# Optimization experiments

Measured on AMD Instinct MI355X. Metric: run time of the kernel, lower is better.

Reference implementation:

```python
import jax, jax.numpy as jnp
import numpy as np

NUM_HEADS = 16
HEAD_DIM = 64
HIDDEN = NUM_HEADS * HEAD_DIM
LN_EPS = 1e-6


def setup_inputs() -> dict:
    key = jax.random.key(0)
    ks = jax.random.split(key, 5)
    B, T, H = 2, 2048, HIDDEN
    s = 1.0 / np.sqrt(H)
    return {
        "h": jax.random.normal(ks[0], (B, T, H), jnp.float32),
        "Wq": jax.random.normal(ks[1], (H, H), jnp.float32) * s,
        "bq": jnp.zeros((H,), jnp.float32),
        "Wk": jax.random.normal(ks[2], (H, H), jnp.float32) * s,
        "bk": jnp.zeros((H,), jnp.float32),
        "Wv": jax.random.normal(ks[3], (H, H), jnp.float32) * s,
        "bv": jnp.zeros((H,), jnp.float32),
        "Wo": jax.random.normal(ks[4], (H, H), jnp.float32) * s,
        "bo": jnp.zeros((H,), jnp.float32),
        "gamma": jnp.ones((H,), jnp.float32),
        "beta": jnp.zeros((H,), jnp.float32),
    }


def _split_heads(x):
    B, T, H = x.shape
    return x.reshape(B, T, NUM_HEADS, HEAD_DIM).transpose(0, 2, 1, 3)  # [B,h,T,d]


def reference(h, Wq, bq, Wk, bk, Wv, bv, Wo, bo, gamma, beta):
    # QKV projections (nn.Linear: x @ W^T + b)
    Q = _split_heads(h @ Wq.T + bq)
    K = _split_heads(h @ Wk.T + bk)
    V = _split_heads(h @ Wv.T + bv)
    scale = HEAD_DIM ** -0.5
    scores = jnp.einsum("bhqd,bhkd->bhqk", Q, K) * scale  # [B,h,T,T]
    attn = jax.nn.softmax(scores, axis=-1)
    ctx = jnp.einsum("bhqk,bhkd->bhqd", attn, V)          # [B,h,T,d]
    B, _, T, _ = ctx.shape
    ctx = ctx.transpose(0, 2, 1, 3).reshape(B, T, HIDDEN)
    out = ctx @ Wo.T + bo + h  # dropout is identity at eval
    # LayerNorm(eps=1e-6)
    mu = out.mean(-1, keepdims=True)
    var = jnp.mean((out - mu) ** 2, -1, keepdims=True)
    return (out - mu) * jax.lax.rsqrt(var + LN_EPS) * gamma + beta
```

## Files before the change

### kernel.cpp

```cpp
#include <hip/hip_runtime.h>
#include <hip/hip_bf16.h>

#define NH   16
#define HD   64
#define HID  1024
#define TSEQ 2048
#define BATCH 2
#define KSCALE 0.18033688011112042f

typedef __attribute__((ext_vector_type(4))) float f32x4;
typedef __attribute__((ext_vector_type(8))) short s16x8;
typedef __attribute__((ext_vector_type(4))) short s16x4;
typedef __attribute__((ext_vector_type(8))) _Float16 f16x8;
typedef __attribute__((ext_vector_type(4))) _Float16 f16x4;
typedef __attribute__((ext_vector_type(2))) _Float16 f16x2;

__device__ __forceinline__ unsigned short f2bf(float f) {
  union { float f; unsigned int u; } v; v.f = f;
  unsigned int r = v.u + 0x7fffu + ((v.u >> 16) & 1u);
  return (unsigned short)(r >> 16);
}
__device__ __forceinline__ float bf2f(unsigned short b) {
  union { unsigned int u; float f; } v; v.u = ((unsigned int)b) << 16; return v.f;
}

__device__ __forceinline__ void gll16(const void* g, void* l) {
  __builtin_amdgcn_global_load_lds(
      (const __attribute__((address_space(1))) unsigned int*)g,
      (__attribute__((address_space(3))) unsigned int*)l, 16, 0, 0);
}

#define WAITBAR(N)                                                      \
  do {                                                                  \
    __builtin_amdgcn_sched_barrier(0);                                  \
    asm volatile("s_waitcnt vmcnt(" #N ")\n\ts_barrier" ::: "memory");  \
  } while (0)

__global__ __launch_bounds__(256) void cast_all_k(
    const float* __restrict__ h,
    const float* __restrict__ w0, const float* __restrict__ w1,
    const float* __restrict__ w2, const float* __restrict__ w3,
    unsigned short* __restrict__ hb, unsigned short* __restrict__ wbase) {
  int i = blockIdx.x * 256 + threadIdx.x;
  const float* src; unsigned short* dst; int idx; float sc = 1.f;
  if (i < 1048576) { src = h; dst = hb; idx = i; }
  else {
    int idx4 = i - 1048576;
    int w = idx4 >> 18;
    idx = idx4 & 262143;
    src = (w == 0) ? w0 : (w == 1) ? w1 : (w == 2) ? w2 : w3;
    dst = wbase + (size_t)(idx4 - idx) * 4;
    if (w == 1) sc = KSCALE;
  }
  float4 v = ((const float4*)src)[idx];
  ushort4 o;
  o.x = f2bf(v.x * sc); o.y = f2bf(v.y * sc); o.z = f2bf(v.z * sc); o.w = f2bf(v.w * sc);
  ((ushort4*)dst)[idx] = o;
}

__global__ __launch_bounds__(256) void gemm_qkv(
    const unsigned short* __restrict__ hb,
    const unsigned short* __restrict__ wcat,
    const float* __restrict__ bq, const float* __restrict__ bk, const float* __restrict__ bv,
    unsigned short* __restrict__ qo, unsigned short* __restrict__ ko,
    unsigned short* __restrict__ vto) {
  __shared__ unsigned short Ash[4][128 * 32];
  __shared__ unsigned short Bsh[4][192 * 32];
  const int tid = threadIdx.x, lane = tid & 63, wave = tid >> 6;
  const int l15 = lane & 15, quad = lane >> 4;
  const int wr = wave >> 1, wc = wave & 1;
  const int bid = blockIdx.y * 16 + blockIdx.x;
  const int swz = (bid & 7) * 64 + (bid >> 3);
  const int bn = (swz & 15) * 192, bm = (swz >> 4) * 128;
  const char* Ab = (const char*)(hb + (size_t)bm * HID);
  const char* Bb = (const char*)(wcat + (size_t)bn * HID);
  const int off = tid * 16;
  const int r0 = off >> 6, c0 = off & 63;
  const size_t ga0 = (size_t)r0 * (HID * 2) + c0;
  const size_t ga1 = ga0 + (size_t)64  * (HID * 2);
  const size_t gb2 = ga0 + (size_t)128 * (HID * 2);
  const int lb0 = wave * 512;
  const int lb1 = 2048 + wave * 512;
  const int lb2 = 4096 + wave * 512;

  f32x4 acc[4][6];
#pragma unroll
  for (int i = 0; i < 4; ++i)
#pragma unroll
    for (int j = 0; j < 6; ++j) acc[i][j] = f32x4{0.f, 0.f, 0.f, 0.f};

  auto stage = [&](int bufi, int k0) {
    const size_t kb = (size_t)k0 * 2;
    gll16(Ab + ga0 + kb, &Ash[bufi][lb0]);
    gll16(Ab + ga1 + kb, &Ash[bufi][lb1]);
    gll16(Bb + ga0 + kb, &Bsh[bufi][lb0]);
    gll16(Bb + ga1 + kb, &Bsh[bufi][lb1]);
    gll16(Bb + gb2 + kb, &Bsh[bufi][lb2]);
  };
  auto compute = [&](int bufi) {
    s16x8 af[4], bfr[6];
#pragma unroll
    for (int i = 0; i < 4; ++i)
      af[i] = *(const s16x8*)(&Ash[bufi][(wr * 64 + i * 16 + l15) * 32 + quad * 8]);
#pragma unroll
    for (int j = 0; j < 6; ++j)
      bfr[j] = *(const s16x8*)(&Bsh[bufi][(wc * 96 + j * 16 + l15) * 32 + quad * 8]);
#pragma unroll
    for (int i = 0; i < 4; ++i)
#pragma unroll
      for (int j = 0; j < 6; ++j)
        acc[i][j] = __builtin_amdgcn_mfma_f32_16x16x32_bf16(af[i], bfr[j], acc[i][j], 0, 0, 0);
  };

  stage(0, 0);
  stage(1, 32);
  stage(2, 64);
  int cur = 0, pf = 3;
  const int NT = HID / 32;
  for (int t = 0; t < NT - 3; ++t) {
    WAITBAR(10);
    stage(pf, (t + 3) * 32);
    compute(cur);
    cur = (cur + 1) & 3;
    pf  = (pf + 1) & 3;
  }
  WAITBAR(10); compute(cur); cur = (cur + 1) & 3;
  WAITBAR(5);  compute(cur); cur = (cur + 1) & 3;
  WAITBAR(0);  compute(cur);

  const int rbase = bm + wr * 64;
#pragma unroll
  for (int j = 0; j < 6; ++j) {
    const int cg  = bn + wc * 96 + j * 16;
    const int mat = cg >> 10;
    const int coln = (cg & 1023) + l15;
    const int head = coln >> 6, d = coln & 63;
    if (mat == 2) {
      const float bb = bv[coln];
#pragma unroll
      for (int i = 0; i < 4; ++i) {
        const int row0 = rbase + i * 16 + quad * 4;
        const int bI = row0 >> 11, t0 = row0 & 2047;
        unsigned short o[4];
#pragma unroll
        for (int r = 0; r < 4; ++r) {
          _Float16 hv = (_Float16)(acc[i][j][r] + bb);
          o[r] = __builtin_bit_cast(unsigned short, hv);
        }
        *(s16x4*)(vto + ((size_t)((bI * NH + head) * HD + d)) * TSEQ + t0) = *(const s16x4*)o;
      }
    } else {
      unsigned short* dst = (mat == 0) ? qo : ko;
      const float bb = (mat == 0) ? bq[coln] : bk[coln] * KSCALE;
#pragma unroll
      for (int i = 0; i < 4; ++i) {
#pragma unroll
        for (int r = 0; r < 4; ++r) {
          const int row = rbase + i * 16 + quad * 4 + r;
          const int bI = row >> 11, t = row & 2047;
          dst[(((size_t)(bI * NH + head) * TSEQ) + t) * HD + d] = f2bf(acc[i][j][r] + bb);
        }
      }
    }
  }
}

__global__ __launch_bounds__(256) void gemm_out(
    const unsigned short* __restrict__ ctx, const unsigned short* __restrict__ wo,
    const float* __restrict__ bo, const float* __restrict__ hres,
    float* __restrict__ outf) {
  __shared__ unsigned short Ash[5][128 * 32];
  __shared__ unsigned short Bsh[5][64 * 32];
  const int tid = threadIdx.x, lane = tid & 63, wave = tid >> 6;
  const int l15 = lane & 15, quad = lane >> 4;
  const int wr = wave >> 1, wc = wave & 1;
  const int bid = blockIdx.y * 16 + blockIdx.x;
  const int swz = (bid & 7) * 64 + (bid >> 3);
  const int bn = (swz & 15) * 64, bm = (swz >> 4) * 128;
  const char* Ab = (const char*)(ctx + (size_t)bm * HID);
  const char* Bb = (const char*)(wo + (size_t)bn * HID);
  const int off = tid * 16;
  const int r0 = off >> 6, c0 = off & 63;
  const size_t ga0 = (size_t)r0 * (HID * 2) + c0;
  const size_t ga1 = ga0 + (size_t)64 * (HID * 2);
  const int lb0 = wave * 512, lb1 = 2048 + wave * 512;

  f32x4 acc[4][2];
#pragma unroll
  for (int i = 0; i < 4; ++i)
#pragma unroll
    for (int j = 0; j < 2; ++j) acc[i][j] = f32x4{0.f, 0.f, 0.f, 0.f};

  auto stage = [&](int bufi, int k0) {
    const size_t kb = (size_t)k0 * 2;
    gll16(Ab + ga0 + kb, &Ash[bufi][lb0]);
    gll16(Ab + ga1 + kb, &Ash[bufi][lb1]);
    gll16(Bb + ga0 + kb, &Bsh[bufi][lb0]);
  };
  auto compute = [&](int bufi) {
    s16x8 af[4], bfr[2];
#pragma unroll
    for (int i = 0; i < 4; ++i)
      af[i] = *(const s16x8*)(&Ash[bufi][(wr * 64 + i * 16 + l15) * 32 + quad * 8]);
#pragma unroll
    for (int j = 0; j < 2; ++j)
      bfr[j] = *(const s16x8*)(&Bsh[bufi][(wc * 32 + j * 16 + l15) * 32 + quad * 8]);
#pragma unroll
    for (int i = 0; i < 4; ++i)
#pragma unroll
      for (int j = 0; j < 2; ++j)
        acc[i][j] = __builtin_amdgcn_mfma_f32_16x16x32_bf16(af[i], bfr[j], acc[i][j], 0, 0, 0);
  };

  stage(0, 0);
  stage(1, 32);
  stage(2, 64);
  stage(3, 96);
  int cur = 0, pf = 4;
  const int NT = HID / 32;
  for (int t = 0; t < NT - 4; ++t) {
    WAITBAR(9);
    stage(pf, (t + 4) * 32);
    compute(cur);
    cur = (cur == 4) ? 0 : cur + 1;
    pf  = (pf  == 4) ? 0 : pf + 1;
  }
  WAITBAR(9); compute(cur); cur = (cur == 4) ? 0 : cur + 1;
  WAITBAR(6); compute(cur); cur = (cur == 4) ? 0 : cur + 1;
  WAITBAR(3); compute(cur); cur = (cur == 4) ? 0 : cur + 1;
  WAITBAR(0); compute(cur);

#pragma unroll
  for (int j = 0; j < 2; ++j) {
    const int col = bn + wc * 32 + j * 16 + l15;
    const float bb = bo[col];
#pragma unroll
    for (int i = 0; i < 4; ++i) {
#pragma unroll
      for (int r = 0; r < 4; ++r) {
        const int row = bm + wr * 64 + i * 16 + quad * 4 + r;
        const size_t o = (size_t)row * HID + col;
        outf[o] = acc[i][j][r] + bb + hres[o];
      }
    }
  }
}

__global__ __launch_bounds__(256, 2) void attn_k(
    const unsigned short* __restrict__ qb, const unsigned short* __restrict__ kb,
    const unsigned short* __restrict__ vt, unsigned short* __restrict__ ctx,
    int ntiles) {
  __shared__ unsigned short Ksh[2][64 * 72];
  __shared__ unsigned short Vsh[2][64 * 72];

  const int tid = threadIdx.x, lane = tid & 63, wave = tid >> 6;
  const int l15 = lane & 15, quad = lane >> 4;
  const int b = blockIdx.z;
  const int h = blockIdx.y, qt = blockIdx.x;
  const size_t ho = ((size_t)(b * NH + h)) * TSEQ * HD;
  const unsigned short* Qh = qb + ho;
  const unsigned short* Kh = kb + ho;
  const unsigned short* Vh = vt + ho;
  const int q0 = qt * 128 + wave * 32;

  s16x8 qf[2][2];
#pragma unroll
  for (int s = 0; s < 2; ++s)
#pragma unroll
    for (int ks = 0; ks < 2; ++ks)
      qf[s][ks] = *(const s16x8*)(Qh + (size_t)(q0 + s * 16 + l15) * HD + ks * 32 + quad * 8);

  f32x4 accO[4][2];
  f32x4 accR[2];
#pragma unroll
  for (int n2 = 0; n2 < 4; ++n2)
#pragma unroll
    for (int s = 0; s < 2; ++s) accO[n2][s] = f32x4{0.f, 0.f, 0.f, 0.f};
  accR[0] = accR[1] = f32x4{0.f, 0.f, 0.f, 0.f};
  const f16x8 vones = {(_Float16)1.f, (_Float16)1.f, (_Float16)1.f, (_Float16)1.f,
                       (_Float16)1.f, (_Float16)1.f, (_Float16)1.f, (_Float16)1.f};

  const int sr = tid >> 3, sc = (tid & 7) * 8;
  const int c = tid & 7;
  const int vwb = (c >> 2) * 32 + (c & 1) * 16 + ((c & 3) >> 1) * 4;
  s16x8 kreg[2], vreg[2];

  auto ldregs = [&](int kt) {
    const int k0n = kt * 64;
#pragma unroll
    for (int hf = 0; hf < 2; ++hf) {
      kreg[hf] = *(const s16x8*)(Kh + (size_t)(k0n + sr + hf * 32) * HD + sc);
      vreg[hf] = *(const s16x8*)(Vh + (size_t)(sr + hf * 32) * TSEQ + k0n + sc);
    }
  };
  auto wlds = [&](int bi) {
#pragma unroll
    for (int hf = 0; hf < 2; ++hf) {
      *(s16x8*)(Ksh[bi] + (sr + hf * 32) * 72 + sc) = kreg[hf];
      const s16x4* vh = (const s16x4*)&vreg[hf];
      *(s16x4*)(Vsh[bi] + (sr + hf * 32) * 72 + vwb)     = vh[0];
      *(s16x4*)(Vsh[bi] + (sr + hf * 32) * 72 + vwb + 8) = vh[1];
    }
  };

  f32x4 accS[2][4];
  f16x4 pP[2][4];

  auto qkt = [&](int bi) {
#pragma unroll
    for (int s = 0; s < 2; ++s)
#pragma unroll
      for (int n = 0; n < 4; ++n) accS[s][n] = f32x4{0.f, 0.f, 0.f, 0.f};
    __builtin_amdgcn_s_setprio(1);
#pragma unroll
    for (int ks = 0; ks < 2; ++ks) {
#pragma unroll
      for (int n = 0; n < 4; ++n) {
        s16x8 kf = *(const s16x8*)(Ksh[bi] + (n * 16 + l15) * 72 + ks * 32 + quad * 8);
#pragma unroll
        for (int s = 0; s < 2; ++s)
          accS[s][n] = __builtin_amdgcn_mfma_f32_16x16x32_bf16(kf, qf[s][ks], accS[s][n], 0, 0, 0);
      }
    }
    __builtin_amdgcn_s_setprio(0);
  };
  auto expp = [&]() {
#pragma unroll
    for (int s = 0; s < 2; ++s)
#pragma unroll
      for (int n = 0; n < 4; ++n) {
        float e0 = __builtin_amdgcn_exp2f(accS[s][n][0]);
        float e1 = __builtin_amdgcn_exp2f(accS[s][n][1]);
        float e2 = __builtin_amdgcn_exp2f(accS[s][n][2]);
        float e3 = __builtin_amdgcn_exp2f(accS[s][n][3]);
        f16x2 lo = __builtin_bit_cast(f16x2, __builtin_amdgcn_cvt_pkrtz(e0, e1));
        f16x2 hi = __builtin_bit_cast(f16x2, __builtin_amdgcn_cvt_pkrtz(e2, e3));
        pP[s][n] = f16x4{lo[0], lo[1], hi[0], hi[1]};
      }
  };
  auto pv = [&](int bi) {
    __builtin_amdgcn_s_setprio(1);
#pragma unroll
    for (int kk = 0; kk < 2; ++kk) {
      union { f16x4 h[2]; f16x8 v8; } u0, u1;
      u0.h[0] = pP[0][2 * kk]; u0.h[1] = pP[0][2 * kk + 1];
      u1.h[0] = pP[1][2 * kk]; u1.h[1] = pP[1][2 * kk + 1];
      accR[0] = __builtin_amdgcn_mfma_f32_16x16x32_f16(vones, u0.v8, accR[0], 0, 0, 0);
      accR[1] = __builtin_amdgcn_mfma_f32_16x16x32_f16(vones, u1.v8, accR[1], 0, 0, 0);
#pragma unroll
      for (int n2 = 0; n2 < 4; ++n2) {
        f16x8 vA = *(const f16x8*)(Vsh[bi] + (n2 * 16 + l15) * 72 + kk * 32 + quad * 8);
        accO[n2][0] = __builtin_amdgcn_mfma_f32_16x16x32_f16(vA, u0.v8, accO[n2][0], 0, 0, 0);
        accO[n2][1] = __builtin_amdgcn_mfma_f32_16x16x32_f16(vA, u1.v8, accO[n2][1], 0, 0, 0);
      }
    }
    __builtin_amdgcn_s_setprio(0);
  };

  ldregs(0);
  wlds(0);
  __syncthreads();
  if (ntiles > 1) ldregs(1);
  qkt(0);
  expp();

  for (int t = 0; t < ntiles - 1; ++t) {
    const int b0 = t & 1, b1 = (t + 1) & 1;
    __syncthreads();
    wlds(b1);
    __syncthreads();
    if (t + 2 < ntiles) ldregs(t + 2);
    qkt(b1);
    pv(b0);
    expp();
  }
  pv((ntiles - 1) & 1);

  float rsum[2] = {accR[0][0], accR[1][0]};

#pragma unroll
  for (int s = 0; s < 2; ++s) {
    const int t = q0 + s * 16 + l15;
    const float inv = 1.f / rsum[s];
#pragma unroll
    for (int n2 = 0; n2 < 4; ++n2) {
      const int d0 = n2 * 16 + quad * 4;
      unsigned short o[4];
#pragma unroll
      for (int r = 0; r < 4; ++r) o[r] = f2bf(accO[n2][s][r] * inv);
      *(s16x4*)(ctx + ((size_t)(b * TSEQ + t)) * HID + h * HD + d0) = *(const s16x4*)o;
    }
  }
}

__global__ __launch_bounds__(256) void ln_k(float* __restrict__ io,
                                            const float* __restrict__ gamma,
                                            const float* __restrict__ beta) {
  const int row = blockIdx.x, tid = threadIdx.x;
  float x[4]; float s = 0.f, s2 = 0.f;
#pragma unroll
  for (int i = 0; i < 4; ++i) {
    x[i] = io[(size_t)row * HID + tid + i * 256];
    s += x[i]; s2 += x[i] * x[i];
  }
#pragma unroll
  for (int off = 1; off < 64; off <<= 1) {
    s  += __shfl_xor(s, off, 64);
    s2 += __shfl_xor(s2, off, 64);
  }
  __shared__ float red[8];
  const int wave = tid >> 6;
  if ((tid & 63) == 0) { red[wave] = s; red[wave + 4] = s2; }
  __syncthreads();
  s  = red[0] + red[1] + red[2] + red[3];
  s2 = red[4] + red[5] + red[6] + red[7];
  const float mean = s * (1.f / HID);
  const float var  = s2 * (1.f / HID) - mean * mean;
  const float rstd = rsqrtf(var + 1e-6f);
#pragma unroll
  for (int i = 0; i < 4; ++i) {
    const int col = tid + i * 256;
    io[(size_t)row * HID + col] = (x[i] - mean) * rstd * gamma[col] + beta[col];
  }
}

extern "C" void kernel_launch(void* const* d_in, const int* in_sizes, int n_in,
                              void* d_out, int out_size, void* d_ws, size_t ws_size,
                              hipStream_t stream) {
  const float* h    = (const float*)d_in[0];
  const float* Wq   = (const float*)d_in[1];
  const float* bq   = (const float*)d_in[2];
  const float* Wk   = (const float*)d_in[3];
  const float* bk   = (const float*)d_in[4];
  const float* Wv   = (const float*)d_in[5];
  const float* bv   = (const float*)d_in[6];
  const float* Wo   = (const float*)d_in[7];
  const float* bo   = (const float*)d_in[8];
  const float* gamma = (const float*)d_in[9];
  const float* beta  = (const float*)d_in[10];
  float* out = (float*)d_out;

  unsigned short* hb   = (unsigned short*)d_ws;
  unsigned short* wqb  = hb  + 4194304;
  unsigned short* wkb  = wqb + 1048576;
  unsigned short* wvb  = wkb + 1048576;
  unsigned short* wob  = wvb + 1048576;
  unsigned short* qb   = wob + 1048576;
  unsigned short* kb   = qb  + 4194304;
  unsigned short* vtf  = kb  + 4194304;
  unsigned short* ctxb = hb;

  cast_all_k<<<8192, 256, 0, stream>>>(h, Wq, Wk, Wv, Wo, hb, wqb);
  gemm_qkv<<<dim3(16, 32), 256, 0, stream>>>(hb, wqb, bq, bk, bv, qb, kb, vtf);
  attn_k<<<dim3(TSEQ / 128, NH, BATCH), 256, 0, stream>>>(qb, kb, vtf, ctxb, 32);
  gemm_out<<<dim3(16, 32), 256, 0, stream>>>(ctxb, wob, bo, h, out);
  ln_k<<<4096, 256, 0, stream>>>(out, gamma, beta);
}
```

Baseline: 200.5 us.

## Fuse LayerNorm into out-projection via last-block counters; shrink attention query tile

The separate LayerNorm kernel is removed. Each gemm_out block now bumps a per-row-panel atomic counter, and the last of the 16 column blocks to finish applies LayerNorm over its 128 rows in place, with counters zeroed in the cast kernel. Separately, the attention query tile is halved from 128 to 64 rows (16 per wave instead of 32), doubling the grid and cutting per-wave registers. The trade is that each K/V tile loaded into LDS is now reused by half as many queries, and the fused LayerNorm runs serially inside the one block that finishes last for each panel.

```diff
diff --git a/kernel.cpp b/kernel.cpp
--- a/kernel.cpp
+++ b/kernel.cpp
@@ -40,7 +40,9 @@
     const float* __restrict__ h,
     const float* __restrict__ w0, const float* __restrict__ w1,
     const float* __restrict__ w2, const float* __restrict__ w3,
-    unsigned short* __restrict__ hb, unsigned short* __restrict__ wbase) {
+    unsigned short* __restrict__ hb, unsigned short* __restrict__ wbase,
+    unsigned int* __restrict__ cnt) {
+  if (blockIdx.x == 0 && threadIdx.x < 32) cnt[threadIdx.x] = 0;
   int i = blockIdx.x * 256 + threadIdx.x;
   const float* src; unsigned short* dst; int idx; float sc = 1.f;
   if (i < 1048576) { src = h; dst = hb; idx = i; }
@@ -168,7 +170,8 @@
 __global__ __launch_bounds__(256) void gemm_out(
     const unsigned short* __restrict__ ctx, const unsigned short* __restrict__ wo,
     const float* __restrict__ bo, const float* __restrict__ hres,
-    float* __restrict__ outf) {
+    float* __restrict__ outf, unsigned int* __restrict__ cnt,
+    const float* __restrict__ gamma, const float* __restrict__ beta) {
   __shared__ unsigned short Ash[5][128 * 32];
   __shared__ unsigned short Bsh[5][64 * 32];
   const int tid = threadIdx.x, lane = tid & 63, wave = tid >> 6;
@@ -244,6 +247,41 @@
       }
     }
   }
+
+  __threadfence();
+  __shared__ unsigned int lastf;
+  if (tid == 0)
+    lastf = (atomicAdd(&cnt[bm >> 7], 1u) == 15u) ? 1u : 0u;
+  __syncthreads();
+  if (!lastf) return;
+  __threadfence();
+  for (int rr = wave; rr < 128; rr += 4) {
+    float* rp = outf + (size_t)(bm + rr) * HID;
+    f32x4 x[4]; float s = 0.f, s2 = 0.f;
+#pragma unroll
+    for (int i = 0; i < 4; ++i) {
+      x[i] = *(const f32x4*)(rp + lane * 4 + i * 256);
+#pragma unroll
+      for (int r = 0; r < 4; ++r) { s += x[i][r]; s2 += x[i][r] * x[i][r]; }
+    }
+#pragma unroll
+    for (int o2 = 1; o2 < 64; o2 <<= 1) {
+      s  += __shfl_xor(s, o2, 64);
+      s2 += __shfl_xor(s2, o2, 64);
+    }
+    const float mean = s * (1.f / HID);
+    const float var  = s2 * (1.f / HID) - mean * mean;
+    const float rstd = rsqrtf(var + 1e-6f);
+#pragma unroll
+    for (int i = 0; i < 4; ++i) {
+      f32x4 g  = *(const f32x4*)(gamma + lane * 4 + i * 256);
+      f32x4 be = *(const f32x4*)(beta  + lane * 4 + i * 256);
+      f32x4 o;
+#pragma unroll
+      for (int r = 0; r < 4; ++r) o[r] = (x[i][r] - mean) * rstd * g[r] + be[r];
+      *(f32x4*)(rp + lane * 4 + i * 256) = o;
+    }
+  }
 }
 
 __global__ __launch_bounds__(256, 2) void attn_k(
@@ -261,22 +299,18 @@
   const unsigned short* Qh = qb + ho;
   const unsigned short* Kh = kb + ho;
   const unsigned short* Vh = vt + ho;
-  const int q0 = qt * 128 + wave * 32;
-
-  s16x8 qf[2][2];
-#pragma unroll
-  for (int s = 0; s < 2; ++s)
-#pragma unroll
-    for (int ks = 0; ks < 2; ++ks)
-      qf[s][ks] = *(const s16x8*)(Qh + (size_t)(q0 + s * 16 + l15) * HD + ks * 32 + quad * 8);
-
-  f32x4 accO[4][2];
-  f32x4 accR[2];
-#pragma unroll
-  for (int n2 = 0; n2 < 4; ++n2)
-#pragma unroll
-    for (int s = 0; s < 2; ++s) accO[n2][s] = f32x4{0.f, 0.f, 0.f, 0.f};
-  accR[0] = accR[1] = f32x4{0.f, 0.f, 0.f, 0.f};
+  const int q0 = qt * 64 + wave * 16;
+
+  s16x8 qf[2];
+#pragma unroll
+  for (int ks = 0; ks < 2; ++ks)
+    qf[ks] = *(const s16x8*)(Qh + (size_t)(q0 + l15) * HD + ks * 32 + quad * 8);
+
+  f32x4 accO[4];
+  f32x4 accR;
+#pragma unroll
+  for (int n2 = 0; n2 < 4; ++n2) accO[n2] = f32x4{0.f, 0.f, 0.f, 0.f};
+  accR = f32x4{0.f, 0.f, 0.f, 0.f};
   const f16x8 vones = {(_Float16)1.f, (_Float16)1.f, (_Float16)1.f, (_Float16)1.f,
                        (_Float16)1.f, (_Float16)1.f, (_Float16)1.f, (_Float16)1.f};
 
@@ -303,55 +337,46 @@
     }
   };
 
-  f32x4 accS[2][4];
-  f16x4 pP[2][4];
+  f32x4 accS[4];
+  f16x4 pP[4];
 
   auto qkt = [&](int bi) {
 #pragma unroll
-    for (int s = 0; s < 2; ++s)
-#pragma unroll
-      for (int n = 0; n < 4; ++n) accS[s][n] = f32x4{0.f, 0.f, 0.f, 0.f};
+    for (int n = 0; n < 4; ++n) accS[n] = f32x4{0.f, 0.f, 0.f, 0.f};
     __builtin_amdgcn_s_setprio(1);
 #pragma unroll
     for (int ks = 0; ks < 2; ++ks) {
 #pragma unroll
       for (int n = 0; n < 4; ++n) {
         s16x8 kf = *(const s16x8*)(Ksh[bi] + (n * 16 + l15) * 72 + ks * 32 + quad * 8);
-#pragma unroll
-        for (int s = 0; s < 2; ++s)
-          accS[s][n] = __builtin_amdgcn_mfma_f32_16x16x32_bf16(kf, qf[s][ks], accS[s][n], 0, 0, 0);
+        accS[n] = __builtin_amdgcn_mfma_f32_16x16x32_bf16(kf, qf[ks], accS[n], 0, 0, 0);
       }
     }
     __builtin_amdgcn_s_setprio(0);
   };
   auto expp = [&]() {
 #pragma unroll
-    for (int s = 0; s < 2; ++s)
-#pragma unroll
-      for (int n = 0; n < 4; ++n) {
-        float e0 = __builtin_amdgcn_exp2f(accS[s][n][0]);
-        float e1 = __builtin_amdgcn_exp2f(accS[s][n][1]);
-        float e2 = __builtin_amdgcn_exp2f(accS[s][n][2]);
-        float e3 = __builtin_amdgcn_exp2f(accS[s][n][3]);
-        f16x2 lo = __builtin_bit_cast(f16x2, __builtin_amdgcn_cvt_pkrtz(e0, e1));
-        f16x2 hi = __builtin_bit_cast(f16x2, __builtin_amdgcn_cvt_pkrtz(e2, e3));
-        pP[s][n] = f16x4{lo[0], lo[1], hi[0], hi[1]};
-      }
+    for (int n = 0; n < 4; ++n) {
+      float e0 = __builtin_amdgcn_exp2f(accS[n][0]);
+      float e1 = __builtin_amdgcn_exp2f(accS[n][1]);
+      float e2 = __builtin_amdgcn_exp2f(accS[n][2]);
+      float e3 = __builtin_amdgcn_exp2f(accS[n][3]);
+      f16x2 lo = __builtin_bit_cast(f16x2, __builtin_amdgcn_cvt_pkrtz(e0, e1));
+      f16x2 hi = __builtin_bit_cast(f16x2, __builtin_amdgcn_cvt_pkrtz(e2, e3));
+      pP[n] = f16x4{lo[0], lo[1], hi[0], hi[1]};
+    }
   };
   auto pv = [&](int bi) {
     __builtin_amdgcn_s_setprio(1);
 #pragma unroll
     for (int kk = 0; kk < 2; ++kk) {
-      union { f16x4 h[2]; f16x8 v8; } u0, u1;
-      u0.h[0] = pP[0][2 * kk]; u0.h[1] = pP[0][2 * kk + 1];
-      u1.h[0] = pP[1][2 * kk]; u1.h[1] = pP[1][2 * kk + 1];
-      accR[0] = __builtin_amdgcn_mfma_f32_16x16x32_f16(vones, u0.v8, accR[0], 0, 0, 0);
-      accR[1] = __builtin_amdgcn_mfma_f32_16x16x32_f16(vones, u1.v8, accR[1], 0, 0, 0);
+      union { f16x4 h[2]; f16x8 v8; } u;
+      u.h[0] = pP[2 * kk]; u.h[1] = pP[2 * kk + 1];
+      accR = __builtin_amdgcn_mfma_f32_16x16x32_f16(vones, u.v8, accR, 0, 0, 0);
 #pragma unroll
       for (int n2 = 0; n2 < 4; ++n2) {
         f16x8 vA = *(const f16x8*)(Vsh[bi] + (n2 * 16 + l15) * 72 + kk * 32 + quad * 8);
-        accO[n2][0] = __builtin_amdgcn_mfma_f32_16x16x32_f16(vA, u0.v8, accO[n2][0], 0, 0, 0);
-        accO[n2][1] = __builtin_amdgcn_mfma_f32_16x16x32_f16(vA, u1.v8, accO[n2][1], 0, 0, 0);
+        accO[n2] = __builtin_amdgcn_mfma_f32_16x16x32_f16(vA, u.v8, accO[n2], 0, 0, 0);
       }
     }
     __builtin_amdgcn_s_setprio(0);
@@ -376,51 +401,15 @@
   }
   pv((ntiles - 1) & 1);
 
-  float rsum[2] = {accR[0][0], accR[1][0]};
-
-#pragma unroll
-  for (int s = 0; s < 2; ++s) {
-    const int t = q0 + s * 16 + l15;
-    const float inv = 1.f / rsum[s];
-#pragma unroll
-    for (int n2 = 0; n2 < 4; ++n2) {
-      const int d0 = n2 * 16 + quad * 4;
-      unsigned short o[4];
-#pragma unroll
-      for (int r = 0; r < 4; ++r) o[r] = f2bf(accO[n2][s][r] * inv);
-      *(s16x4*)(ctx + ((size_t)(b * TSEQ + t)) * HID + h * HD + d0) = *(const s16x4*)o;
-    }
-  }
-}
-
-__global__ __launch_bounds__(256) void ln_k(float* __restrict__ io,
-                                            const float* __restrict__ gamma,
-                                            const float* __restrict__ beta) {
-  const int row = blockIdx.x, tid = threadIdx.x;
-  float x[4]; float s = 0.f, s2 = 0.f;
-#pragma unroll
-  for (int i = 0; i < 4; ++i) {
-    x[i] = io[(size_t)row * HID + tid + i * 256];
-    s += x[i]; s2 += x[i] * x[i];
-  }
-#pragma unroll
-  for (int off = 1; off < 64; off <<= 1) {
-    s  += __shfl_xor(s, off, 64);
-    s2 += __shfl_xor(s2, off, 64);
-  }
-  __shared__ float red[8];
-  const int wave = tid >> 6;
-  if ((tid & 63) == 0) { red[wave] = s; red[wave + 4] = s2; }
-  __syncthreads();
-  s  = red[0] + red[1] + red[2] + red[3];
-  s2 = red[4] + red[5] + red[6] + red[7];
-  const float mean = s * (1.f / HID);
-  const float var  = s2 * (1.f / HID) - mean * mean;
-  const float rstd = rsqrtf(var + 1e-6f);
-#pragma unroll
-  for (int i = 0; i < 4; ++i) {
-    const int col = tid + i * 256;
-    io[(size_t)row * HID + col] = (x[i] - mean) * rstd * gamma[col] + beta[col];
+  const float inv = 1.f / accR[0];
+  const int tq = q0 + l15;
+#pragma unroll
+  for (int n2 = 0; n2 < 4; ++n2) {
+    const int d0 = n2 * 16 + quad * 4;
+    unsigned short o[4];
+#pragma unroll
+    for (int r = 0; r < 4; ++r) o[r] = f2bf(accO[n2][r] * inv);
+    *(s16x4*)(ctx + ((size_t)(b * TSEQ + tq)) * HID + h * HD + d0) = *(const s16x4*)o;
   }
 }
 
@@ -449,10 +438,10 @@
   unsigned short* kb   = qb  + 4194304;
   unsigned short* vtf  = kb  + 4194304;
   unsigned short* ctxb = hb;
-
-  cast_all_k<<<8192, 256, 0, stream>>>(h, Wq, Wk, Wv, Wo, hb, wqb);
+  unsigned int* cnt    = (unsigned int*)(vtf + 4194304);
+
+  cast_all_k<<<8192, 256, 0, stream>>>(h, Wq, Wk, Wv, Wo, hb, wqb, cnt);
   gemm_qkv<<<dim3(16, 32), 256, 0, stream>>>(hb, wqb, bq, bk, bv, qb, kb, vtf);
-  attn_k<<<dim3(TSEQ / 128, NH, BATCH), 256, 0, stream>>>(qb, kb, vtf, ctxb, 32);
-  gemm_out<<<dim3(16, 32), 256, 0, stream>>>(ctxb, wob, bo, h, out);
-  ln_k<<<4096, 256, 0, stream>>>(out, gamma, beta);
-}
+  attn_k<<<dim3(TSEQ / 64, NH, BATCH), 256, 0, stream>>>(qb, kb, vtf, ctxb, 32);
+  gemm_out<<<dim3(16, 32), 256, 0, stream>>>(ctxb, wob, bo, h, out, cnt, gamma, beta);
+}
```

Result: slower. 297.6 us (+48.4%).
